# Optimization experiments

Hardware: AMD Instinct MI355X
Metric: run time of the kernel (lower is better)

Reference implementation:

```python
import jax, jax.numpy as jnp
import numpy as np

B, S, D, H = 4, 2048, 1024, 16
DK = D // H  # 64


def setup_inputs() -> dict:
    key = jax.random.key(0)
    ks = jax.random.split(key, 11)
    scale = 1.0 / np.sqrt(D)
    inp = {
        "query": jax.random.normal(ks[0], (B, S, D), jnp.float32),
        "key": jax.random.normal(ks[1], (B, S, D), jnp.float32),
        "value": jax.random.normal(ks[2], (B, S, D), jnp.float32),
        "Wq": jax.random.normal(ks[3], (D, D), jnp.float32) * scale,
        "bq": jnp.zeros((D,), jnp.float32),
        "Wk": jax.random.normal(ks[4], (D, D), jnp.float32) * scale,
        "bk": jnp.zeros((D,), jnp.float32),
        "Wv": jax.random.normal(ks[5], (D, D), jnp.float32) * scale,
        "bv": jnp.zeros((D,), jnp.float32),
        "Wo": jax.random.normal(ks[6], (D, D), jnp.float32) * scale,
        "bo": jnp.zeros((D,), jnp.float32),
    }
    return inp


def reference(query, key, value, Wq, bq, Wk, bk, Wv, bv, Wo, bo):
    # Projections: torch Linear computes x @ W.T + b; here W is stored as (in, out)
    def split_heads(x):
        return x.reshape(B, S, H, DK).transpose(0, 2, 1, 3)  # [B,H,S,DK]

    Q = split_heads(query @ Wq + bq)
    K = split_heads(key @ Wk + bk)
    V = split_heads(value @ Wv + bv)

    scores = jnp.einsum("bhqd,bhkd->bhqk", Q, K) / jnp.sqrt(jnp.float32(DK))
    attn = jax.nn.softmax(scores, axis=-1)  # [B,H,S,S]
    ctx = jnp.einsum("bhqk,bhkd->bhqd", attn, V)
    ctx = ctx.transpose(0, 2, 1, 3).reshape(B, S, D)
    return ctx @ Wo + bo
```

## Files before the change

kernel.cpp:

```cpp
#include <hip/hip_runtime.h>
#include <hip/hip_bf16.h>
#include <cstdint>

#define DEV __device__ __forceinline__

typedef __bf16 bf16x8 __attribute__((ext_vector_type(8)));
typedef float f32x4 __attribute__((ext_vector_type(4)));
typedef unsigned short u16;
typedef unsigned short u16x8 __attribute__((ext_vector_type(8)));
typedef unsigned short u16x4 __attribute__((ext_vector_type(4)));

#if defined(__has_builtin) && __has_builtin(__builtin_amdgcn_exp2f)
#define EXP2F(x) __builtin_amdgcn_exp2f(x)
#else
#define EXP2F(x) exp2f(x)
#endif

static constexpr float QSCALE = 0.125f * 1.44269504088896340736f;

DEV u16 f2bf(float f) {
  uint32_t x = __builtin_bit_cast(uint32_t, f);
  x += 0x7fffu + ((x >> 16) & 1u);
  return (u16)(x >> 16);
}

DEV u16x4 pack4(float a, float b, float c, float d) {
  union { __hip_bfloat162 h[2]; u16x4 u; } r;
  r.h[0] = __float22bfloat162_rn(make_float2(a, b));
  r.h[1] = __float22bfloat162_rn(make_float2(c, d));
  return r.u;
}

DEV u16x8 cvt8(const float* p) {
  const float4 v0 = *(const float4*)p;
  const float4 v1 = *(const float4*)(p + 4);
  union { __hip_bfloat162 h[4]; u16x8 u; } r;
  r.h[0] = __float22bfloat162_rn(make_float2(v0.x, v0.y));
  r.h[1] = __float22bfloat162_rn(make_float2(v0.z, v0.w));
  r.h[2] = __float22bfloat162_rn(make_float2(v1.x, v1.y));
  r.h[3] = __float22bfloat162_rn(make_float2(v1.z, v1.w));
  return r.u;
}

DEV f32x4 mfma16(bf16x8 a, bf16x8 b, f32x4 c) {
  return __builtin_amdgcn_mfma_f32_16x16x32_bf16(a, b, c, 0, 0, 0);
}

DEV void gll16(const void* g, const void* l) {
  __builtin_amdgcn_global_load_lds(
      (const __attribute__((address_space(1))) uint32_t*)g,
      (__attribute__((address_space(3))) uint32_t*)l, 16, 0, 0);
}

__global__ __launch_bounds__(256) void cvt_kernel(
    const float* __restrict__ X0, const float* __restrict__ X1,
    const float* __restrict__ X2, u16* __restrict__ Y0,
    u16* __restrict__ Y1, u16* __restrict__ Y2) {
  const float* X = (blockIdx.z == 0) ? X0 : (blockIdx.z == 1) ? X1 : X2;
  u16* Y = (blockIdx.z == 0) ? Y0 : (blockIdx.z == 1) ? Y1 : Y2;
  const size_t i = ((size_t)blockIdx.x * 256 + threadIdx.x) * 8;
  *(u16x8*)(Y + i) = cvt8(X + i);
}

__global__ __launch_bounds__(256) void wtrans_kernel(
    const float* __restrict__ W0, const float* __restrict__ W1,
    const float* __restrict__ W2, const float* __restrict__ W3,
    u16* __restrict__ T0, u16* __restrict__ T1,
    u16* __restrict__ T2, u16* __restrict__ T3) {
  const float* W = (blockIdx.z == 0) ? W0 : (blockIdx.z == 1) ? W1 : (blockIdx.z == 2) ? W2 : W3;
  u16* T = (blockIdx.z == 0) ? T0 : (blockIdx.z == 1) ? T1 : (blockIdx.z == 2) ? T2 : T3;
  __shared__ float tile[32][33];
  const int tid = threadIdx.x;
  const int r = tid >> 3, c0 = (tid & 7) * 4;
  const float4 v = *(const float4*)(W + (size_t)(blockIdx.y * 32 + r) * 1024 + blockIdx.x * 32 + c0);
  tile[r][c0 + 0] = v.x; tile[r][c0 + 1] = v.y; tile[r][c0 + 2] = v.z; tile[r][c0 + 3] = v.w;
  __syncthreads();
  u16x4 o = pack4(tile[c0 + 0][r], tile[c0 + 1][r], tile[c0 + 2][r], tile[c0 + 3][r]);
  *(u16x4*)(T + (size_t)(blockIdx.x * 32 + r) * 1024 + blockIdx.y * 32 + c0) = o;
}

template <int EPI>
__global__ __launch_bounds__(512) void gemm_kernel(
    const u16* __restrict__ X, const u16* __restrict__ Wt,
    const float* __restrict__ bias, void* __restrict__ OutV, float scale) {
  __shared__ u16 As[128 * 32];
  __shared__ u16 Bs[128 * 32];
  const int tid = threadIdx.x;
  const int w = tid >> 6, lane = tid & 63, ln = lane & 15, quad = lane >> 4;
  const int wm = w >> 1, wn = w & 1;
  const int bm = blockIdx.y * 128, bn = blockIdx.x * 128;

  f32x4 acc[2][4];
#pragma unroll
  for (int i = 0; i < 2; i++)
#pragma unroll
    for (int j = 0; j < 4; j++) acc[i][j] = f32x4{0.f, 0.f, 0.f, 0.f};

  const int lrow = w * 16 + (lane >> 2);
  const u16* ga = X + (size_t)(bm + lrow) * 1024 + (lane & 3) * 8;
  const u16* gb = Wt + (size_t)(bn + lrow) * 1024 + (lane & 3) * 8;
  const u16* lA = As + w * 512;
  const u16* lB = Bs + w * 512;

  for (int kt = 0; kt < 32; ++kt) {
    __syncthreads();
    gll16(ga + kt * 32, lA);
    gll16(gb + kt * 32, lB);
    __syncthreads();

    bf16x8 af[2], bf[4];
#pragma unroll
    for (int i = 0; i < 2; i++) af[i] = *(const bf16x8*)&As[(wm * 32 + i * 16 + ln) * 32 + quad * 8];
#pragma unroll
    for (int j = 0; j < 4; j++) bf[j] = *(const bf16x8*)&Bs[(wn * 64 + j * 16 + ln) * 32 + quad * 8];
#pragma unroll
    for (int i = 0; i < 2; i++)
#pragma unroll
      for (int j = 0; j < 4; j++) acc[i][j] = mfma16(af[i], bf[j], acc[i][j]);
  }

#pragma unroll
  for (int j = 0; j < 4; j++) {
    const int n = bn + wn * 64 + j * 16 + ln;
    const float bv = bias[n];
#pragma unroll
    for (int i = 0; i < 2; i++) {
      const int m0 = bm + wm * 32 + i * 16 + quad * 4;
      if (EPI == 0) {
        u16* O = (u16*)OutV;
        const int h = n >> 6, dk = n & 63;
#pragma unroll
        for (int r = 0; r < 4; r++) {
          const int m = m0 + r, b = m >> 11, s = m & 2047;
          O[((size_t)(b * 16 + h) * 2048 + s) * 64 + dk] = f2bf((acc[i][j][r] + bv) * scale);
        }
      } else if (EPI == 2) {
        u16* O = (u16*)OutV;
        const int b = m0 >> 11, s0 = m0 & 2047, h = n >> 6, dk = n & 63;
        u16x4 pk = pack4((acc[i][j][0] + bv) * scale, (acc[i][j][1] + bv) * scale,
                         (acc[i][j][2] + bv) * scale, (acc[i][j][3] + bv) * scale);
        *(u16x4*)(O + (size_t)((b * 16 + h) * 64 + dk) * 2048 + s0) = pk;
      } else {
        float* O = (float*)OutV;
#pragma unroll
        for (int r = 0; r < 4; r++) O[(size_t)(m0 + r) * 1024 + n] = acc[i][j][r] + bv;
      }
    }
  }
}

__global__ __launch_bounds__(256) void fattn_kernel(
    const u16* __restrict__ Q, const u16* __restrict__ K,
    const u16* __restrict__ V, u16* __restrict__ ctx) {
  __shared__ u16 Ks[64 * 64];
  __shared__ u16 Vs[64 * 64];
  __shared__ u16 Ps[4 * 32 * 64];

  const int tid = threadIdx.x;
  const int w = tid >> 6, lane = tid & 63, ln = lane & 15, quad = lane >> 4;
  const int qt = blockIdx.x, bh = blockIdx.y;
  const size_t base = (size_t)bh * 2048 * 64;

  const int sr0 = tid >> 3, sc = (tid & 7) * 8;
  const int sr1 = 32 + sr0;
  const int swc = (((tid & 7) ^ (sr0 & 7))) * 8;
  const int sw = ln & 7;

  bf16x8 qf[2][2];
#pragma unroll
  for (int j = 0; j < 2; j++)
#pragma unroll
    for (int ks = 0; ks < 2; ks++)
      qf[j][ks] = *(const bf16x8*)(Q + base + (size_t)(qt * 128 + w * 32 + j * 16 + ln) * 64 + ks * 32 + quad * 8);

  f32x4 lv[2];
  lv[0] = f32x4{0.f, 0.f, 0.f, 0.f};
  lv[1] = f32x4{0.f, 0.f, 0.f, 0.f};
  f32x4 accO[4][2];
#pragma unroll
  for (int d = 0; d < 4; d++)
#pragma unroll
    for (int j = 0; j < 2; j++) accO[d][j] = f32x4{0.f, 0.f, 0.f, 0.f};

  u16x8 kr0, kr1, vr0, vr1;
  kr0 = *(const u16x8*)(K + base + (size_t)sr0 * 64 + sc);
  kr1 = *(const u16x8*)(K + base + (size_t)sr1 * 64 + sc);
  vr0 = *(const u16x8*)(V + base + (size_t)sr0 * 2048 + sc);
  vr1 = *(const u16x8*)(V + base + (size_t)sr1 * 2048 + sc);

  for (int t = 0; t < 32; ++t) {
    __syncthreads();
    *(u16x8*)&Ks[sr0 * 64 + swc] = kr0;
    *(u16x8*)&Ks[sr1 * 64 + swc] = kr1;
    *(u16x8*)&Vs[sr0 * 64 + swc] = vr0;
    *(u16x8*)&Vs[sr1 * 64 + swc] = vr1;
    __syncthreads();

    if (t < 31) {
      const int tn = t + 1;
      kr0 = *(const u16x8*)(K + base + (size_t)(tn * 64 + sr0) * 64 + sc);
      kr1 = *(const u16x8*)(K + base + (size_t)(tn * 64 + sr1) * 64 + sc);
      vr0 = *(const u16x8*)(V + base + (size_t)sr0 * 2048 + tn * 64 + sc);
      vr1 = *(const u16x8*)(V + base + (size_t)sr1 * 2048 + tn * 64 + sc);
    }

    f32x4 s[4][2];
#pragma unroll
    for (int i = 0; i < 4; i++)
#pragma unroll
      for (int j = 0; j < 2; j++) s[i][j] = f32x4{0.f, 0.f, 0.f, 0.f};
    __builtin_amdgcn_s_setprio(1);
#pragma unroll
    for (int i = 0; i < 4; i++) {
#pragma unroll
      for (int ks = 0; ks < 2; ks++) {
        const bf16x8 kf = *(const bf16x8*)&Ks[(i * 16 + ln) * 64 + ((4 * ks + quad) ^ sw) * 8];
        s[i][0] = mfma16(kf, qf[0][ks], s[i][0]);
        s[i][1] = mfma16(kf, qf[1][ks], s[i][1]);
      }
    }
    __builtin_amdgcn_s_setprio(0);

#pragma unroll
    for (int j = 0; j < 2; j++) {
#pragma unroll
      for (int i = 0; i < 4; i++) {
#pragma unroll
        for (int r = 0; r < 4; r++) s[i][j][r] = EXP2F(s[i][j][r]);
        lv[j] += s[i][j];
        *(u16x4*)&Ps[(w * 32 + j * 16 + ln) * 64 +
                     (((2 * i + (quad >> 1)) ^ sw) * 8) + (quad & 1) * 4] =
            pack4(s[i][j][0], s[i][j][1], s[i][j][2], s[i][j][3]);
      }
    }

    __builtin_amdgcn_s_setprio(1);
#pragma unroll
    for (int ks = 0; ks < 2; ks++) {
      const bf16x8 pf0 = *(const bf16x8*)&Ps[(w * 32 + 0 * 16 + ln) * 64 + ((4 * ks + quad) ^ sw) * 8];
      const bf16x8 pf1 = *(const bf16x8*)&Ps[(w * 32 + 1 * 16 + ln) * 64 + ((4 * ks + quad) ^ sw) * 8];
#pragma unroll
      for (int dkt = 0; dkt < 4; dkt++) {
        const bf16x8 vf = *(const bf16x8*)&Vs[(dkt * 16 + ln) * 64 + ((4 * ks + quad) ^ sw) * 8];
        accO[dkt][0] = mfma16(vf, pf0, accO[dkt][0]);
        accO[dkt][1] = mfma16(vf, pf1, accO[dkt][1]);
      }
    }
    __builtin_amdgcn_s_setprio(0);
  }

  const int b = bh >> 4, h = bh & 15;
#pragma unroll
  for (int j = 0; j < 2; j++) {
    float l = (lv[j][0] + lv[j][1]) + (lv[j][2] + lv[j][3]);
    l += __shfl_xor(l, 16, 64);
    l += __shfl_xor(l, 32, 64);
    const float linv = 1.0f / l;
    const int qs = qt * 128 + w * 32 + j * 16 + ln;
#pragma unroll
    for (int dkt = 0; dkt < 4; dkt++) {
      u16x4 pk = pack4(accO[dkt][j][0] * linv, accO[dkt][j][1] * linv,
                       accO[dkt][j][2] * linv, accO[dkt][j][3] * linv);
      *(u16x4*)(ctx + (size_t)(b * 2048 + qs) * 1024 + h * 64 + dkt * 16 + quad * 4) = pk;
    }
  }
}

extern "C" void kernel_launch(void* const* d_in, const int* in_sizes, int n_in,
                              void* d_out, int out_size, void* d_ws, size_t ws_size,
                              hipStream_t stream) {
  const float* q  = (const float*)d_in[0];
  const float* k  = (const float*)d_in[1];
  const float* v  = (const float*)d_in[2];
  const float* Wq = (const float*)d_in[3];
  const float* bq = (const float*)d_in[4];
  const float* Wk = (const float*)d_in[5];
  const float* bk = (const float*)d_in[6];
  const float* Wv = (const float*)d_in[7];
  const float* bv = (const float*)d_in[8];
  const float* Wo = (const float*)d_in[9];
  const float* bo = (const float*)d_in[10];

  u16* Wtq = (u16*)d_ws;
  u16* Wtk = Wtq + 1024 * 1024;
  u16* Wtv = Wtk + 1024 * 1024;
  u16* Wto = Wtv + 1024 * 1024;
  u16* qb  = Wto + 1024 * 1024;
  u16* kb  = qb + 8192 * 1024;
  u16* vb  = kb + 8192 * 1024;
  u16* Qb  = vb + 8192 * 1024;
  u16* Kb  = Qb + 8192 * 1024;
  u16* Vtb = Kb + 8192 * 1024;
  u16* Cb  = qb;

  cvt_kernel<<<dim3(4096, 1, 3), 256, 0, stream>>>(q, k, v, qb, kb, vb);
  wtrans_kernel<<<dim3(32, 32, 4), 256, 0, stream>>>(Wq, Wk, Wv, Wo, Wtq, Wtk, Wtv, Wto);

  const dim3 gg(8, 64);
  gemm_kernel<0><<<gg, 512, 0, stream>>>(qb, Wtq, bq, Qb, QSCALE);
  gemm_kernel<0><<<gg, 512, 0, stream>>>(kb, Wtk, bk, Kb, 1.0f);
  gemm_kernel<2><<<gg, 512, 0, stream>>>(vb, Wtv, bv, Vtb, 1.0f);

  fattn_kernel<<<dim3(16, 64), 256, 0, stream>>>(Qb, Kb, Vtb, Cb);

  gemm_kernel<3><<<gg, 512, 0, stream>>>(Cb, Wto, bo, d_out, 1.0f);
}
```

Baseline: 373.8 us.

## Batch QKV GEMMs into one launch and split attention across eight waves

The three separate Q/K/V projection GEMM launches become one gemm_qkv_kernel that picks its operands by blockIdx.z, so launches are fewer and the three GEMMs fill the GPU together. The attention kernel now runs 512 threads per block: each wave handles 16 query rows instead of 32 and each thread stages one K/V row instead of two. This halves per-wave register state and raises wave-level parallelism for latency hiding, but each wave reuses every K/V LDS fragment half as often, so LDS reads per MFMA roughly double.

New measurement: 364.3 us. -2.5%, faster.

```diff
diff --git a/kernel.cpp b/kernel.cpp
--- a/kernel.cpp
+++ b/kernel.cpp
@@ -79,10 +79,83 @@
   *(u16x4*)(T + (size_t)(blockIdx.x * 32 + r) * 1024 + blockIdx.y * 32 + c0) = o;
 }
 
-template <int EPI>
-__global__ __launch_bounds__(512) void gemm_kernel(
+__global__ __launch_bounds__(512) void gemm_qkv_kernel(
+    const u16* __restrict__ X0, const u16* __restrict__ X1,
+    const u16* __restrict__ X2, const u16* __restrict__ W0t,
+    const u16* __restrict__ W1t, const u16* __restrict__ W2t,
+    const float* __restrict__ b0, const float* __restrict__ b1,
+    const float* __restrict__ b2, u16* __restrict__ O0,
+    u16* __restrict__ O1, u16* __restrict__ O2) {
+  __shared__ u16 As[128 * 32];
+  __shared__ u16 Bs[128 * 32];
+  const int z = blockIdx.z;
+  const u16* X = (z == 0) ? X0 : (z == 1) ? X1 : X2;
+  const u16* Wt = (z == 0) ? W0t : (z == 1) ? W1t : W2t;
+  const float* bias = (z == 0) ? b0 : (z == 1) ? b1 : b2;
+  u16* O = (z == 0) ? O0 : (z == 1) ? O1 : O2;
+  const float scale = (z == 0) ? QSCALE : 1.0f;
+
+  const int tid = threadIdx.x;
+  const int w = tid >> 6, lane = tid & 63, ln = lane & 15, quad = lane >> 4;
+  const int wm = w >> 1, wn = w & 1;
+  const int bm = blockIdx.y * 128, bn = blockIdx.x * 128;
+
+  f32x4 acc[2][4];
+#pragma unroll
+  for (int i = 0; i < 2; i++)
+#pragma unroll
+    for (int j = 0; j < 4; j++) acc[i][j] = f32x4{0.f, 0.f, 0.f, 0.f};
+
+  const int lrow = w * 16 + (lane >> 2);
+  const u16* ga = X + (size_t)(bm + lrow) * 1024 + (lane & 3) * 8;
+  const u16* gb = Wt + (size_t)(bn + lrow) * 1024 + (lane & 3) * 8;
+  const u16* lA = As + w * 512;
+  const u16* lB = Bs + w * 512;
+
+  for (int kt = 0; kt < 32; ++kt) {
+    __syncthreads();
+    gll16(ga + kt * 32, lA);
+    gll16(gb + kt * 32, lB);
+    __syncthreads();
+
+    bf16x8 af[2], bf[4];
+#pragma unroll
+    for (int i = 0; i < 2; i++) af[i] = *(const bf16x8*)&As[(wm * 32 + i * 16 + ln) * 32 + quad * 8];
+#pragma unroll
+    for (int j = 0; j < 4; j++) bf[j] = *(const bf16x8*)&Bs[(wn * 64 + j * 16 + ln) * 32 + quad * 8];
+#pragma unroll
+    for (int i = 0; i < 2; i++)
+#pragma unroll
+      for (int j = 0; j < 4; j++) acc[i][j] = mfma16(af[i], bf[j], acc[i][j]);
+  }
+
+#pragma unroll
+  for (int j = 0; j < 4; j++) {
+    const int n = bn + wn * 64 + j * 16 + ln;
+    const float bv = bias[n];
+#pragma unroll
+    for (int i = 0; i < 2; i++) {
+      const int m0 = bm + wm * 32 + i * 16 + quad * 4;
+      const int h = n >> 6, dk = n & 63;
+      if (z != 2) {
+#pragma unroll
+        for (int r = 0; r < 4; r++) {
+          const int m = m0 + r, b = m >> 11, s = m & 2047;
+          O[((size_t)(b * 16 + h) * 2048 + s) * 64 + dk] = f2bf((acc[i][j][r] + bv) * scale);
+        }
+      } else {
+        const int b = m0 >> 11, s0 = m0 & 2047;
+        u16x4 pk = pack4(acc[i][j][0] + bv, acc[i][j][1] + bv,
+                         acc[i][j][2] + bv, acc[i][j][3] + bv);
+        *(u16x4*)(O + (size_t)((b * 16 + h) * 64 + dk) * 2048 + s0) = pk;
+      }
+    }
+  }
+}
+
+__global__ __launch_bounds__(512) void gemm_o_kernel(
     const u16* __restrict__ X, const u16* __restrict__ Wt,
-    const float* __restrict__ bias, void* __restrict__ OutV, float scale) {
+    const float* __restrict__ bias, float* __restrict__ Out) {
   __shared__ u16 As[128 * 32];
   __shared__ u16 Bs[128 * 32];
   const int tid = threadIdx.x;
@@ -126,143 +199,101 @@
 #pragma unroll
     for (int i = 0; i < 2; i++) {
       const int m0 = bm + wm * 32 + i * 16 + quad * 4;
-      if (EPI == 0) {
-        u16* O = (u16*)OutV;
-        const int h = n >> 6, dk = n & 63;
-#pragma unroll
-        for (int r = 0; r < 4; r++) {
-          const int m = m0 + r, b = m >> 11, s = m & 2047;
-          O[((size_t)(b * 16 + h) * 2048 + s) * 64 + dk] = f2bf((acc[i][j][r] + bv) * scale);
-        }
-      } else if (EPI == 2) {
-        u16* O = (u16*)OutV;
-        const int b = m0 >> 11, s0 = m0 & 2047, h = n >> 6, dk = n & 63;
-        u16x4 pk = pack4((acc[i][j][0] + bv) * scale, (acc[i][j][1] + bv) * scale,
-                         (acc[i][j][2] + bv) * scale, (acc[i][j][3] + bv) * scale);
-        *(u16x4*)(O + (size_t)((b * 16 + h) * 64 + dk) * 2048 + s0) = pk;
-      } else {
-        float* O = (float*)OutV;
-#pragma unroll
-        for (int r = 0; r < 4; r++) O[(size_t)(m0 + r) * 1024 + n] = acc[i][j][r] + bv;
-      }
-    }
-  }
-}
-
-__global__ __launch_bounds__(256) void fattn_kernel(
+#pragma unroll
+      for (int r = 0; r < 4; r++) Out[(size_t)(m0 + r) * 1024 + n] = acc[i][j][r] + bv;
+    }
+  }
+}
+
+__global__ __launch_bounds__(512) void fattn_kernel(
     const u16* __restrict__ Q, const u16* __restrict__ K,
     const u16* __restrict__ V, u16* __restrict__ ctx) {
   __shared__ u16 Ks[64 * 64];
   __shared__ u16 Vs[64 * 64];
-  __shared__ u16 Ps[4 * 32 * 64];
+  __shared__ u16 Ps[8 * 16 * 64];
 
   const int tid = threadIdx.x;
   const int w = tid >> 6, lane = tid & 63, ln = lane & 15, quad = lane >> 4;
   const int qt = blockIdx.x, bh = blockIdx.y;
   const size_t base = (size_t)bh * 2048 * 64;
 
-  const int sr0 = tid >> 3, sc = (tid & 7) * 8;
-  const int sr1 = 32 + sr0;
-  const int swc = (((tid & 7) ^ (sr0 & 7))) * 8;
+  const int sr = tid >> 3, sc = (tid & 7) * 8;
+  const int swc = ((tid & 7) ^ (sr & 7)) * 8;
   const int sw = ln & 7;
 
-  bf16x8 qf[2][2];
-#pragma unroll
-  for (int j = 0; j < 2; j++)
-#pragma unroll
-    for (int ks = 0; ks < 2; ks++)
-      qf[j][ks] = *(const bf16x8*)(Q + base + (size_t)(qt * 128 + w * 32 + j * 16 + ln) * 64 + ks * 32 + quad * 8);
-
-  f32x4 lv[2];
-  lv[0] = f32x4{0.f, 0.f, 0.f, 0.f};
-  lv[1] = f32x4{0.f, 0.f, 0.f, 0.f};
-  f32x4 accO[4][2];
-#pragma unroll
-  for (int d = 0; d < 4; d++)
-#pragma unroll
-    for (int j = 0; j < 2; j++) accO[d][j] = f32x4{0.f, 0.f, 0.f, 0.f};
-
-  u16x8 kr0, kr1, vr0, vr1;
-  kr0 = *(const u16x8*)(K + base + (size_t)sr0 * 64 + sc);
-  kr1 = *(const u16x8*)(K + base + (size_t)sr1 * 64 + sc);
-  vr0 = *(const u16x8*)(V + base + (size_t)sr0 * 2048 + sc);
-  vr1 = *(const u16x8*)(V + base + (size_t)sr1 * 2048 + sc);
+  bf16x8 qf[2];
+#pragma unroll
+  for (int ks = 0; ks < 2; ks++)
+    qf[ks] = *(const bf16x8*)(Q + base + (size_t)(qt * 128 + w * 16 + ln) * 64 + ks * 32 + quad * 8);
+
+  f32x4 lv = f32x4{0.f, 0.f, 0.f, 0.f};
+  f32x4 accO[4];
+#pragma unroll
+  for (int d = 0; d < 4; d++) accO[d] = f32x4{0.f, 0.f, 0.f, 0.f};
+
+  u16x8 kr = *(const u16x8*)(K + base + (size_t)sr * 64 + sc);
+  u16x8 vr = *(const u16x8*)(V + base + (size_t)sr * 2048 + sc);
 
   for (int t = 0; t < 32; ++t) {
     __syncthreads();
-    *(u16x8*)&Ks[sr0 * 64 + swc] = kr0;
-    *(u16x8*)&Ks[sr1 * 64 + swc] = kr1;
-    *(u16x8*)&Vs[sr0 * 64 + swc] = vr0;
-    *(u16x8*)&Vs[sr1 * 64 + swc] = vr1;
+    *(u16x8*)&Ks[sr * 64 + swc] = kr;
+    *(u16x8*)&Vs[sr * 64 + swc] = vr;
     __syncthreads();
 
     if (t < 31) {
       const int tn = t + 1;
-      kr0 = *(const u16x8*)(K + base + (size_t)(tn * 64 + sr0) * 64 + sc);
-      kr1 = *(const u16x8*)(K + base + (size_t)(tn * 64 + sr1) * 64 + sc);
-      vr0 = *(const u16x8*)(V + base + (size_t)sr0 * 2048 + tn * 64 + sc);
-      vr1 = *(const u16x8*)(V + base + (size_t)sr1 * 2048 + tn * 64 + sc);
-    }
-
-    f32x4 s[4][2];
-#pragma unroll
-    for (int i = 0; i < 4; i++)
-#pragma unroll
-      for (int j = 0; j < 2; j++) s[i][j] = f32x4{0.f, 0.f, 0.f, 0.f};
+      kr = *(const u16x8*)(K + base + (size_t)(tn * 64 + sr) * 64 + sc);
+      vr = *(const u16x8*)(V + base + (size_t)sr * 2048 + tn * 64 + sc);
+    }
+
+    f32x4 s[4];
+#pragma unroll
+    for (int i = 0; i < 4; i++) s[i] = f32x4{0.f, 0.f, 0.f, 0.f};
     __builtin_amdgcn_s_setprio(1);
 #pragma unroll
     for (int i = 0; i < 4; i++) {
 #pragma unroll
       for (int ks = 0; ks < 2; ks++) {
         const bf16x8 kf = *(const bf16x8*)&Ks[(i * 16 + ln) * 64 + ((4 * ks + quad) ^ sw) * 8];
-        s[i][0] = mfma16(kf, qf[0][ks], s[i][0]);
-        s[i][1] = mfma16(kf, qf[1][ks], s[i][1]);
+        s[i] = mfma16(kf, qf[ks], s[i]);
       }
     }
     __builtin_amdgcn_s_setprio(0);
 
 #pragma unroll
-    for (int j = 0; j < 2; j++) {
-#pragma unroll
-      for (int i = 0; i < 4; i++) {
-#pragma unroll
-        for (int r = 0; r < 4; r++) s[i][j][r] = EXP2F(s[i][j][r]);
-        lv[j] += s[i][j];
-        *(u16x4*)&Ps[(w * 32 + j * 16 + ln) * 64 +
-                     (((2 * i + (quad >> 1)) ^ sw) * 8) + (quad & 1) * 4] =
-            pack4(s[i][j][0], s[i][j][1], s[i][j][2], s[i][j][3]);
-      }
+    for (int i = 0; i < 4; i++) {
+#pragma unroll
+      for (int r = 0; r < 4; r++) s[i][r] = EXP2F(s[i][r]);
+      lv += s[i];
+      *(u16x4*)&Ps[(w * 16 + ln) * 64 +
+                   (((2 * i + (quad >> 1)) ^ sw) * 8) + (quad & 1) * 4] =
+          pack4(s[i][0], s[i][1], s[i][2], s[i][3]);
     }
 
     __builtin_amdgcn_s_setprio(1);
 #pragma unroll
     for (int ks = 0; ks < 2; ks++) {
-      const bf16x8 pf0 = *(const bf16x8*)&Ps[(w * 32 + 0 * 16 + ln) * 64 + ((4 * ks + quad) ^ sw) * 8];
-      const bf16x8 pf1 = *(const bf16x8*)&Ps[(w * 32 + 1 * 16 + ln) * 64 + ((4 * ks + quad) ^ sw) * 8];
+      const bf16x8 pf = *(const bf16x8*)&Ps[(w * 16 + ln) * 64 + ((4 * ks + quad) ^ sw) * 8];
 #pragma unroll
       for (int dkt = 0; dkt < 4; dkt++) {
         const bf16x8 vf = *(const bf16x8*)&Vs[(dkt * 16 + ln) * 64 + ((4 * ks + quad) ^ sw) * 8];
-        accO[dkt][0] = mfma16(vf, pf0, accO[dkt][0]);
-        accO[dkt][1] = mfma16(vf, pf1, accO[dkt][1]);
+        accO[dkt] = mfma16(vf, pf, accO[dkt]);
       }
     }
     __builtin_amdgcn_s_setprio(0);
   }
 
   const int b = bh >> 4, h = bh & 15;
-#pragma unroll
-  for (int j = 0; j < 2; j++) {
-    float l = (lv[j][0] + lv[j][1]) + (lv[j][2] + lv[j][3]);
-    l += __shfl_xor(l, 16, 64);
-    l += __shfl_xor(l, 32, 64);
-    const float linv = 1.0f / l;
-    const int qs = qt * 128 + w * 32 + j * 16 + ln;
-#pragma unroll
-    for (int dkt = 0; dkt < 4; dkt++) {
-      u16x4 pk = pack4(accO[dkt][j][0] * linv, accO[dkt][j][1] * linv,
-                       accO[dkt][j][2] * linv, accO[dkt][j][3] * linv);
-      *(u16x4*)(ctx + (size_t)(b * 2048 + qs) * 1024 + h * 64 + dkt * 16 + quad * 4) = pk;
-    }
+  float l = (lv[0] + lv[1]) + (lv[2] + lv[3]);
+  l += __shfl_xor(l, 16, 64);
+  l += __shfl_xor(l, 32, 64);
+  const float linv = 1.0f / l;
+  const int qs = qt * 128 + w * 16 + ln;
+#pragma unroll
+  for (int dkt = 0; dkt < 4; dkt++) {
+    u16x4 pk = pack4(accO[dkt][0] * linv, accO[dkt][1] * linv,
+                     accO[dkt][2] * linv, accO[dkt][3] * linv);
+    *(u16x4*)(ctx + (size_t)(b * 2048 + qs) * 1024 + h * 64 + dkt * 16 + quad * 4) = pk;
   }
 }
 
@@ -296,12 +327,10 @@
   cvt_kernel<<<dim3(4096, 1, 3), 256, 0, stream>>>(q, k, v, qb, kb, vb);
   wtrans_kernel<<<dim3(32, 32, 4), 256, 0, stream>>>(Wq, Wk, Wv, Wo, Wtq, Wtk, Wtv, Wto);
 
-  const dim3 gg(8, 64);
-  gemm_kernel<0><<<gg, 512, 0, stream>>>(qb, Wtq, bq, Qb, QSCALE);
-  gemm_kernel<0><<<gg, 512, 0, stream>>>(kb, Wtk, bk, Kb, 1.0f);
-  gemm_kernel<2><<<gg, 512, 0, stream>>>(vb, Wtv, bv, Vtb, 1.0f);
-
-  fattn_kernel<<<dim3(16, 64), 256, 0, stream>>>(Qb, Kb, Vtb, Cb);
-
-  gemm_kernel<3><<<gg, 512, 0, stream>>>(Cb, Wto, bo, d_out, 1.0f);
-}
+  gemm_qkv_kernel<<<dim3(8, 64, 3), 512, 0, stream>>>(
+      qb, kb, vb, Wtq, Wtk, Wtv, bq, bk, bv, Qb, Kb, Vtb);
+
+  fattn_kernel<<<dim3(16, 64), 512, 0, stream>>>(Qb, Kb, Vtb, Cb);
+
+  gemm_o_kernel<<<dim3(8, 64), 512, 0, stream>>>(Cb, Wto, bo, (float*)d_out);
+}
```
